# Kernel optimization log

Hardware: AMD Instinct MI355X
Metric: run time of the kernel (lower is better)

## Reference

```python
import jax, jax.numpy as jnp
import numpy as np

HEADS, K = 8, 32
EPS = 1e-5


def bn(x, gamma, beta):
    # batch-stat BN over all axes except the last (channel) axis
    axes = tuple(range(x.ndim - 1))
    m = jnp.mean(x, axes, keepdims=True)
    v = jnp.var(x, axes, keepdims=True)
    return (x - m) / jnp.sqrt(v + EPS) * gamma + beta


def leaky(z):
    return jax.nn.leaky_relu(z, 0.2)


def conv1(t, W, g, b):  # 1x1 Conv1d + BN + LeakyReLU, channels-last
    return leaky(bn(jnp.einsum('bnc,dc->bnd', t, W), g, b))


def conv2(t, W, g, b):  # 1x1 Conv2d + BN + LeakyReLU on (B,N,k,C)
    return leaky(bn(jnp.einsum('bnkc,dc->bnkd', t, W), g, b))


def _forward(x, pos, Wq, gq, bq, Wk, gk, bk, Wv, gv, bv,
             Wpb, gpb, bpb, We1, ge1, be1, We2, ge2, be2,
             Wm1, gm1, bm1, Wm2, gm2, bm2):
    B, N, C = x.shape
    cph = C // HEADS
    q = conv1(x, Wq, gq, bq)
    key = conv1(x, Wk, gk, bk)
    val = conv1(x, Wv, gv, bv)
    # kNN in key-feature space (DGCNN-style get_graph_feature, edge_function='global')
    sq = jnp.sum(key * key, -1)                          # (B,N)
    dist = sq[:, :, None] + sq[:, None, :] - 2.0 * jnp.einsum('bnc,bmc->bnm', key, key)
    _, idx = jax.lax.top_k(-dist, K)                     # (B,N,K)
    bidx = jnp.arange(B)[:, None, None]
    key_nb = key[bidx, idx]                              # (B,N,K,C)
    val_nb = val[bidx, idx]
    pos_nb = pos[bidx, idx]
    mask = jnp.sign(idx + 1).astype(x.dtype)             # (B,N,K), all ones for valid knn
    masked_pos = (pos_nb - pos[:, :, None, :]) * mask[..., None]
    posb = conv2(masked_pos, Wpb, gpb, bpb)              # (B,N,K,C)
    vector = key_nb - q[:, :, None, :] + posb            # vector attention logits input
    value = val_nb + posb
    vector = conv2(conv2(vector, We1, ge1, be1), We2, ge2, be2)  # (B,N,K,cph)
    vector = jax.nn.softmax(vector, axis=2) * mask[..., None]    # softmax over k neighbors
    value = value.reshape(B, N, K, cph, HEADS)
    attn = jnp.einsum('bnkgh,bnkg->bngh', value, vector).reshape(B, N, C)
    x = x + attn
    h = jax.nn.silu(bn(jnp.einsum('bnc,dc->bnd', x, Wm1), gm1, bm1))
    m = jax.nn.silu(bn(jnp.einsum('bnc,dc->bnd', h, Wm2), gm2, bm2))
    return x + m


def setup_inputs():
    key = jax.random.key(0)
    ks = jax.random.split(key, 16)
    B, N, C, H = 2, 2048, 256, 512
    cph = C // HEADS
    s = 0.02
    inp = {
        'x': jax.random.normal(ks[0], (B, N, C), jnp.float32),
        'pos': jax.random.normal(ks[1], (B, N, C), jnp.float32),
        'Wq': jax.random.normal(ks[2], (C, C), jnp.float32) * s,
        'gq': jnp.ones((C,), jnp.float32), 'bq': jnp.zeros((C,), jnp.float32),
        'Wk': jax.random.normal(ks[3], (C, C), jnp.float32) * s,
        'gk': jnp.ones((C,), jnp.float32), 'bk': jnp.zeros((C,), jnp.float32),
        'Wv': jax.random.normal(ks[4], (C, C), jnp.float32) * s,
        'gv': jnp.ones((C,), jnp.float32), 'bv': jnp.zeros((C,), jnp.float32),
        'Wpb': jax.random.normal(ks[5], (C, C), jnp.float32) * s,
        'gpb': jnp.ones((C,), jnp.float32), 'bpb': jnp.zeros((C,), jnp.float32),
        'We1': jax.random.normal(ks[6], (cph, C), jnp.float32) * s,
        'ge1': jnp.ones((cph,), jnp.float32), 'be1': jnp.zeros((cph,), jnp.float32),
        'We2': jax.random.normal(ks[7], (cph, cph), jnp.float32) * s,
        'ge2': jnp.ones((cph,), jnp.float32), 'be2': jnp.zeros((cph,), jnp.float32),
        'Wm1': jax.random.normal(ks[8], (H, C), jnp.float32) * s,
        'gm1': jnp.ones((H,), jnp.float32), 'bm1': jnp.zeros((H,), jnp.float32),
        'Wm2': jax.random.normal(ks[9], (C, H), jnp.float32) * s,
        'gm2': jnp.ones((C,), jnp.float32), 'bm2': jnp.zeros((C,), jnp.float32),
    }
    return inp


def reference(x, pos, Wq, gq, bq, Wk, gk, bk, Wv, gv, bv,
              Wpb, gpb, bpb, We1, ge1, be1, We2, ge2, be2,
              Wm1, gm1, bm1, Wm2, gm2, bm2):
    return _forward(x, pos, Wq, gq, bq, Wk, gk, bk, Wv, gv, bv,
                    Wpb, gpb, bpb, We1, ge1, be1, We2, ge2, be2,
                    Wm1, gm1, bm1, Wm2, gm2, bm2)
```

## Files before the change

kernel.cpp:

```cpp
#include <hip/hip_runtime.h>

#define EPS 1e-5f

typedef __attribute__((ext_vector_type(8))) short s8v;
typedef __attribute__((ext_vector_type(4))) float f4v;

__device__ __forceinline__ float leakyf(float z){ return z >= 0.f ? z : 0.2f*z; }
__device__ __forceinline__ float siluf(float y){ return y / (1.f + __expf(-y)); }
__device__ __forceinline__ unsigned f2bfu(float f){
  unsigned u = __float_as_uint(f);
  return (u + 0x7FFFu + ((u>>16)&1u)) >> 16;
}
__device__ __forceinline__ unsigned short bfr(float f){ return (unsigned short)f2bfu(f); }
__device__ __forceinline__ float bf2f16(unsigned short s){ return __uint_as_float(((unsigned)s)<<16); }

__global__ __launch_bounds__(256) void k_zero(float* __restrict__ p, int n){
  int i = blockIdx.x*256 + threadIdx.x;
  if (i < n) p[i] = 0.f;
}

template<bool TRANSA, bool STATS>
__global__ __launch_bounds__(256) void k_gemm(
    const float* __restrict__ A, int lda,
    const float* __restrict__ tA, const float* __restrict__ gA, const float* __restrict__ bA, int CA,
    const float* __restrict__ B0, const float* __restrict__ B1, const float* __restrict__ B2,
    int ldb, float* __restrict__ C, int ldc, long cStr, int K,
    float* __restrict__ buck, int statC, int statChanStr)
{
  __shared__ unsigned short Ah[2048], Al[2048], Bh[2048], Bl[2048];
  __shared__ float Ssum[64], Ssq[64];
  const int z = blockIdx.z;
  const float* Bb = (z==0?B0:(z==1?B1:B2));
  float* Cb = C + (long)z*cStr;
  const int tid = threadIdx.x;
  const int bm = blockIdx.x*64, bn = blockIdx.y*64;
  const int wv = tid>>6, lane = tid&63;
  const int lm = lane&15, quad = lane>>4;
  if (STATS && tid<64){ Ssum[tid]=0.f; Ssq[tid]=0.f; }

  const int r0 = tid>>3, kg = tid&7;
  const int qk = kg>>1, j0 = (kg&1)*4;
  const int s0 = ((((r0>>4)  )*4 + qk)*16 + ((r0&15)^qk))*8 + j0;
  const int s1 = ((((r0>>4)+2)*4 + qk)*16 + ((r0&15)^qk))*8 + j0;
  const float* aP0 = A  + (long)(bm+r0)*lda + kg*4;
  const float* aP1 = aP0 + (long)32*lda;
  const float* bP0 = Bb + (long)(bn+r0)*ldb + kg*4;
  const float* bP1 = bP0 + (long)32*ldb;

  f4v acc[4];
  #pragma unroll
  for (int j=0;j<4;j++) acc[j] = (f4v){0.f,0.f,0.f,0.f};

  float4 a0 = *(const float4*)(aP0);
  float4 a1 = *(const float4*)(aP1);
  float4 b0 = *(const float4*)(bP0);
  float4 b1 = *(const float4*)(bP1);

  for (int k0=0; k0<K; k0+=32){
    float4 av0 = a0, av1 = a1;
    if (TRANSA){
      const float* tm = tA + k0 + kg*4;
      float4 m4 = *(const float4*)tm;
      float4 r4 = *(const float4*)(tm + CA);
      float4 g4 = *(const float4*)(gA + k0 + kg*4);
      float4 b4 = *(const float4*)(bA + k0 + kg*4);
      av0.x = siluf((av0.x - m4.x)*r4.x*g4.x + b4.x);
      av0.y = siluf((av0.y - m4.y)*r4.y*g4.y + b4.y);
      av0.z = siluf((av0.z - m4.z)*r4.z*g4.z + b4.z);
      av0.w = siluf((av0.w - m4.w)*r4.w*g4.w + b4.w);
      av1.x = siluf((av1.x - m4.x)*r4.x*g4.x + b4.x);
      av1.y = siluf((av1.y - m4.y)*r4.y*g4.y + b4.y);
      av1.z = siluf((av1.z - m4.z)*r4.z*g4.z + b4.z);
      av1.w = siluf((av1.w - m4.w)*r4.w*g4.w + b4.w);
    }
    ushort4 h4, l4;
    h4.x=bfr(av0.x); l4.x=bfr(av0.x-bf2f16(h4.x));
    h4.y=bfr(av0.y); l4.y=bfr(av0.y-bf2f16(h4.y));
    h4.z=bfr(av0.z); l4.z=bfr(av0.z-bf2f16(h4.z));
    h4.w=bfr(av0.w); l4.w=bfr(av0.w-bf2f16(h4.w));
    *(ushort4*)&Ah[s0]=h4; *(ushort4*)&Al[s0]=l4;
    h4.x=bfr(av1.x); l4.x=bfr(av1.x-bf2f16(h4.x));
    h4.y=bfr(av1.y); l4.y=bfr(av1.y-bf2f16(h4.y));
    h4.z=bfr(av1.z); l4.z=bfr(av1.z-bf2f16(h4.z));
    h4.w=bfr(av1.w); l4.w=bfr(av1.w-bf2f16(h4.w));
    *(ushort4*)&Ah[s1]=h4; *(ushort4*)&Al[s1]=l4;
    h4.x=bfr(b0.x); l4.x=bfr(b0.x-bf2f16(h4.x));
    h4.y=bfr(b0.y); l4.y=bfr(b0.y-bf2f16(h4.y));
    h4.z=bfr(b0.z); l4.z=bfr(b0.z-bf2f16(h4.z));
    h4.w=bfr(b0.w); l4.w=bfr(b0.w-bf2f16(h4.w));
    *(ushort4*)&Bh[s0]=h4; *(ushort4*)&Bl[s0]=l4;
    h4.x=bfr(b1.x); l4.x=bfr(b1.x-bf2f16(h4.x));
    h4.y=bfr(b1.y); l4.y=bfr(b1.y-bf2f16(h4.y));
    h4.z=bfr(b1.z); l4.z=bfr(b1.z-bf2f16(h4.z));
    h4.w=bfr(b1.w); l4.w=bfr(b1.w-bf2f16(h4.w));
    *(ushort4*)&Bh[s1]=h4; *(ushort4*)&Bl[s1]=l4;
    __syncthreads();
    if (k0+32 < K){
      a0 = *(const float4*)(aP0 + k0+32);
      a1 = *(const float4*)(aP1 + k0+32);
      b0 = *(const float4*)(bP0 + k0+32);
      b1 = *(const float4*)(bP1 + k0+32);
    }
    const int soA = ((wv*4 + quad)*16 + (lm^quad))*8;
    s8v ah = *(const s8v*)&Ah[soA];
    s8v al = *(const s8v*)&Al[soA];
    #pragma unroll
    for (int j=0;j<4;j++){
      const int soB = ((j*4 + quad)*16 + (lm^quad))*8;
      s8v bh = *(const s8v*)&Bh[soB];
      s8v bl = *(const s8v*)&Bl[soB];
      acc[j] = __builtin_amdgcn_mfma_f32_16x16x32_bf16(ah, bh, acc[j], 0,0,0);
      acc[j] = __builtin_amdgcn_mfma_f32_16x16x32_bf16(ah, bl, acc[j], 0,0,0);
      acc[j] = __builtin_amdgcn_mfma_f32_16x16x32_bf16(al, bh, acc[j], 0,0,0);
      acc[j] = __builtin_amdgcn_mfma_f32_16x16x32_bf16(al, bl, acc[j], 0,0,0);
    }
    __syncthreads();
  }
  #pragma unroll
  for (int rr=0;rr<4;rr++){
    float* cr = Cb + (long)(bm + wv*16 + quad*4 + rr)*ldc + bn + lm;
    #pragma unroll
    for (int j=0;j<4;j++) cr[j*16] = acc[j][rr];
  }
  if (STATS){
    #pragma unroll
    for (int j=0;j<4;j++){
      float s=0.f, q=0.f;
      #pragma unroll
      for (int rr=0;rr<4;rr++){ float v = acc[j][rr]; s += v; q += v*v; }
      s += __shfl_xor(s,16,64); s += __shfl_xor(s,32,64);
      q += __shfl_xor(q,16,64); q += __shfl_xor(q,32,64);
      if (quad==0){ atomicAdd(&Ssum[j*16+lm], s); atomicAdd(&Ssq[j*16+lm], q); }
    }
    __syncthreads();
    if (tid < 64){
      int chan = statChanStr*z + bn + tid;
      float* bb = buck + (long)(blockIdx.x & 63)*2*statC;
      atomicAdd(&bb[chan], Ssum[tid]);
      atomicAdd(&bb[statC + chan], Ssq[tid]);
    }
  }
}

__global__ void k_finalize(const float* __restrict__ buck, int C, float invn, float* __restrict__ mr){
  int c = blockIdx.x*256 + threadIdx.x;
  if (c < C){
    float s=0,q=0;
    for (int b=0;b<64;b++){ s += buck[(long)b*2*C + c]; q += buck[(long)b*2*C + C + c]; }
    float m = s*invn;
    float v = fmaxf(q*invn - m*m, 0.f);
    mr[c] = m; mr[C+c] = rsqrtf(v + EPS);
  }
}

__global__ __launch_bounds__(256) void k_apply_qkv(const float* __restrict__ raw, const float* __restrict__ mr,
    const float* __restrict__ gq, const float* __restrict__ bq,
    const float* __restrict__ gk, const float* __restrict__ bk,
    const float* __restrict__ gv, const float* __restrict__ bv,
    float* __restrict__ key, float* __restrict__ qv, float* __restrict__ sq){
  const int r = blockIdx.x, tid = threadIdx.x;
  __shared__ float red[256];
  const float* row = raw + (long)r*768;
  float zq = row[tid], zk = row[256+tid], zv = row[512+tid];
  float yq = leakyf((zq - mr[tid])*mr[768+tid]*gq[tid] + bq[tid]);
  float yk = leakyf((zk - mr[256+tid])*mr[1024+tid]*gk[tid] + bk[tid]);
  float yv = leakyf((zv - mr[512+tid])*mr[1280+tid]*gv[tid] + bv[tid]);
  qv[(long)r*512 + tid] = yq;
  key[(long)r*256 + tid] = yk;
  qv[(long)r*512 + 256 + tid] = yv;
  red[tid] = yk*yk; __syncthreads();
  for (int off=128; off; off>>=1){ if (tid<off) red[tid] += red[tid+off]; __syncthreads(); }
  if (tid==0) sq[r] = red[0];
}

__global__ __launch_bounds__(256) void k_topk(const float* __restrict__ G, const float* __restrict__ sqb,
    int* __restrict__ idxb){
  __shared__ float dist[4][2048];
  const int wv = threadIdx.x >> 6, lane = threadIdx.x & 63;
  const int n = blockIdx.x*4 + wv;
  const float* Grow = G + (long)n*2048;
  const float sqn = sqb[n];
  float lmin = 3.4e38f; int lidx = 0;
  for (int j=0;j<32;j++){
    int m = lane + j*64;
    float d = sqn + sqb[m] - 2.f*Grow[m];
    dist[wv][m] = d;
    if (d < lmin){ lmin = d; lidx = m; }
  }
  int* orow = idxb + n*32;
  for (int t=0;t<32;t++){
    float v = lmin; int i = lidx;
    for (int off=32; off; off>>=1){
      float v2 = __shfl_xor(v, off, 64);
      int i2 = __shfl_xor(i, off, 64);
      if (v2 < v || (v2 == v && i2 < i)){ v = v2; i = i2; }
    }
    if (lane == 0) orow[t] = i;
    if ((i & 63) == lane){
      dist[wv][i] = 3.4e38f;
      lmin = 3.4e38f; lidx = 0;
      for (int j=0;j<32;j++){
        int m = lane + j*64;
        float d = dist[wv][m];
        if (d < lmin){ lmin = d; lidx = m; }
      }
    }
  }
}

__global__ __launch_bounds__(256) void k_stats_pb(const float* __restrict__ P, const int* __restrict__ idx,
    float* __restrict__ buck){
  const int c = threadIdx.x;
  float s=0,q=0;
  for (int r = blockIdx.x; r < 4096; r += gridDim.x){
    const long base = (long)(r >> 11) << 11;
    const float pn = P[(long)r*256 + c];
    const int* ir = idx + r*32;
    for (int k=0;k<32;k++){
      int g = ir[k];
      float z = P[(base + g)*256 + c] - pn;
      s += z; q += z*z;
    }
  }
  float* bb = buck + (long)(blockIdx.x & 63)*512;
  atomicAdd(&bb[c], s); atomicAdd(&bb[256+c], q);
}

__global__ __launch_bounds__(256) void k_e1m(
    const float* __restrict__ key, const float* __restrict__ qv, const float* __restrict__ P,
    const int* __restrict__ idx, const float* __restrict__ mrPB,
    const float* __restrict__ gpb, const float* __restrict__ bpb,
    const float* __restrict__ We1, float* __restrict__ E1, float* __restrict__ buckE1)
{
  __shared__ unsigned short Ab[16384];
  __shared__ unsigned short Wb[8192];
  __shared__ float Ssum[32], Ssq[32];
  const int tid = threadIdx.x;
  const int wv = tid>>6, lane = tid&63;
  const int quad = lane>>4, lm = lane&15;
  const int bn0 = blockIdx.x*2;
  if (tid < 32){ Ssum[tid]=0.f; Ssq[tid]=0.f; }
  for (int e = tid; e < 8192; e += 256){
    int d = e >> 8, c = e & 255;
    int off = (((d>>4)*8 + (c>>5))*4 + ((c>>3)&3))*128 + (d&15)*8 + (c&7);
    Wb[off] = bfr(We1[e]);
  }
  {
    const int bn = bn0 + (wv>>1);
    const long base = (long)(bn >> 11) << 11;
    const int c4 = lane*4;
    float4 q4  = *(const float4*)(qv + (long)bn*512 + c4);
    float4 pn4 = *(const float4*)(P + (long)bn*256 + c4);
    float4 mp4 = *(const float4*)(mrPB + c4);
    float4 rp4 = *(const float4*)(mrPB + 256 + c4);
    float4 g4  = *(const float4*)(gpb + c4);
    float4 b4  = *(const float4*)(bpb + c4);
    const int ksc = c4>>5, quadc = (c4>>3)&3, jc = c4&7;
    for (int j = 0; j < 16; ++j){
      const int rloc = wv*16 + j;
      const int kk = rloc & 31;
      const int g = idx[bn*32 + kk];
      float4 kb = *(const float4*)(key + (base+g)*256 + c4);
      float4 pb = *(const float4*)(P + (base+g)*256 + c4);
      float o0 = kb.x - q4.x + leakyf((pb.x - pn4.x - mp4.x)*rp4.x*g4.x + b4.x);
      float o1 = kb.y - q4.y + leakyf((pb.y - pn4.y - mp4.y)*rp4.y*g4.y + b4.y);
      float o2 = kb.z - q4.z + leakyf((pb.z - pn4.z - mp4.z)*rp4.z*g4.z + b4.z);
      float o3 = kb.w - q4.w + leakyf((pb.w - pn4.w - mp4.w)*rp4.w*g4.w + b4.w);
      const int atile = rloc >> 4;
      const int slot = ((rloc & 15) ^ (ksc<<1) ^ quadc) & 15;
      const int off = ((atile*8 + ksc)*4 + quadc)*128 + slot*8 + jc;
      ushort4 u; u.x = bfr(o0); u.y = bfr(o1); u.z = bfr(o2); u.w = bfr(o3);
      *(ushort4*)&Ab[off] = u;
    }
  }
  __syncthreads();
  f4v acc0 = (f4v){0,0,0,0}, acc1 = (f4v){0,0,0,0};
  #pragma unroll
  for (int ks=0; ks<8; ks++){
    const int aslot = (lm ^ (ks<<1) ^ quad) & 15;
    s8v a  = *(const s8v*)&Ab[((wv*8 + ks)*4 + quad)*128 + aslot*8];
    s8v b0 = *(const s8v*)&Wb[((ks)*4 + quad)*128 + lm*8];
    s8v b1 = *(const s8v*)&Wb[((8 + ks)*4 + quad)*128 + lm*8];
    acc0 = __builtin_amdgcn_mfma_f32_16x16x32_bf16(a, b0, acc0, 0,0,0);
    acc1 = __builtin_amdgcn_mfma_f32_16x16x32_bf16(a, b1, acc1, 0,0,0);
  }
  {
    const int bn = bn0 + (wv>>1);
    const int mt = wv & 1;
    #pragma unroll
    for (int rr=0; rr<4; rr++){
      int krow = mt*16 + quad*4 + rr;
      float* o = E1 + ((long)bn*32 + krow)*32;
      o[lm]      = acc0[rr];
      o[16 + lm] = acc1[rr];
    }
  }
  float s0=0,q0=0,s1=0,q1=0;
  #pragma unroll
  for (int rr=0; rr<4; rr++){
    s0 += acc0[rr]; q0 += acc0[rr]*acc0[rr];
    s1 += acc1[rr]; q1 += acc1[rr]*acc1[rr];
  }
  s0 += __shfl_xor(s0,16,64); s0 += __shfl_xor(s0,32,64);
  q0 += __shfl_xor(q0,16,64); q0 += __shfl_xor(q0,32,64);
  s1 += __shfl_xor(s1,16,64); s1 += __shfl_xor(s1,32,64);
  q1 += __shfl_xor(q1,16,64); q1 += __shfl_xor(q1,32,64);
  if (quad == 0){
    atomicAdd(&Ssum[lm], s0);      atomicAdd(&Ssq[lm], q0);
    atomicAdd(&Ssum[16+lm], s1);   atomicAdd(&Ssq[16+lm], q1);
  }
  __syncthreads();
  if (tid < 32){
    float* bb = buckE1 + (long)(blockIdx.x & 63)*64;
    atomicAdd(&bb[tid], Ssum[tid]); atomicAdd(&bb[32+tid], Ssq[tid]);
  }
}

__global__ __launch_bounds__(256) void k_e2m(
    float* __restrict__ E, const float* __restrict__ mrE1,
    const float* __restrict__ ge1, const float* __restrict__ be1,
    const float* __restrict__ We2, float* __restrict__ buckE2)
{
  __shared__ unsigned short Ab[8192];
  __shared__ unsigned short Wb[1024];
  __shared__ float Ssum[32], Ssq[32];
  const int tid = threadIdx.x;
  const int wv = tid>>6, lane = tid&63;
  const int quad = lane>>4, lm = lane&15;
  const long r0 = (long)blockIdx.x*256;
  if (tid < 32){ Ssum[tid]=0.f; Ssq[tid]=0.f; }
  for (int e = tid; e < 1024; e += 256){
    int d = e>>5, c = e&31;
    int off = ((d>>4)*4 + ((c>>3)&3))*128 + (d&15)*8 + (c&7);
    Wb[off] = bfr(We2[e]);
  }
  #pragma unroll
  for (int it=0; it<8; it++){
    int e = (tid + it*256)*4;
    int row = e>>5, c = e&31;
    float4 v = *(const float4*)(E + (r0 + row)*32 + c);
    float4 m4 = *(const float4*)(mrE1 + c);
    float4 r4 = *(const float4*)(mrE1 + 32 + c);
    float4 g4 = *(const float4*)(ge1 + c);
    float4 b4 = *(const float4*)(be1 + c);
    float o0 = leakyf((v.x - m4.x)*r4.x*g4.x + b4.x);
    float o1 = leakyf((v.y - m4.y)*r4.y*g4.y + b4.y);
    float o2 = leakyf((v.z - m4.z)*r4.z*g4.z + b4.z);
    float o3 = leakyf((v.w - m4.w)*r4.w*g4.w + b4.w);
    int quadc = (c>>3)&3, jc = c&7;
    int slot = ((row&15) ^ quadc) & 15;
    int off = ((row>>4)*4 + quadc)*128 + slot*8 + jc;
    ushort4 u; u.x=bfr(o0); u.y=bfr(o1); u.z=bfr(o2); u.w=bfr(o3);
    *(ushort4*)&Ab[off] = u;
  }
  __syncthreads();
  f4v acc0[4], acc1[4];
  #pragma unroll
  for (int i=0;i<4;i++){ acc0[i]=(f4v){0,0,0,0}; acc1[i]=(f4v){0,0,0,0}; }
  const int aslot = (lm ^ quad) & 15;
  s8v b0 = *(const s8v*)&Wb[(quad)*128 + lm*8];
  s8v b1 = *(const s8v*)&Wb[(4 + quad)*128 + lm*8];
  #pragma unroll
  for (int i=0;i<4;i++){
    const int atile = wv*4 + i;
    s8v a = *(const s8v*)&Ab[(atile*4 + quad)*128 + aslot*8];
    acc0[i] = __builtin_amdgcn_mfma_f32_16x16x32_bf16(a, b0, acc0[i], 0,0,0);
    acc1[i] = __builtin_amdgcn_mfma_f32_16x16x32_bf16(a, b1, acc1[i], 0,0,0);
  }
  __syncthreads();
  float s0=0,q0=0,s1=0,q1=0;
  #pragma unroll
  for (int i=0;i<4;i++){
    const int atile = wv*4 + i;
    #pragma unroll
    for (int rr=0; rr<4; rr++){
      long row = r0 + atile*16 + quad*4 + rr;
      float* o = E + row*32;
      o[lm]      = acc0[i][rr];
      o[16 + lm] = acc1[i][rr];
      s0 += acc0[i][rr]; q0 += acc0[i][rr]*acc0[i][rr];
      s1 += acc1[i][rr]; q1 += acc1[i][rr]*acc1[i][rr];
    }
  }
  s0 += __shfl_xor(s0,16,64); s0 += __shfl_xor(s0,32,64);
  q0 += __shfl_xor(q0,16,64); q0 += __shfl_xor(q0,32,64);
  s1 += __shfl_xor(s1,16,64); s1 += __shfl_xor(s1,32,64);
  q1 += __shfl_xor(q1,16,64); q1 += __shfl_xor(q1,32,64);
  if (quad == 0){
    atomicAdd(&Ssum[lm], s0);    atomicAdd(&Ssq[lm], q0);
    atomicAdd(&Ssum[16+lm], s1); atomicAdd(&Ssq[16+lm], q1);
  }
  __syncthreads();
  if (tid < 32){
    float* bb = buckE2 + (long)(blockIdx.x & 63)*64;
    atomicAdd(&bb[tid], Ssum[tid]); atomicAdd(&bb[32+tid], Ssq[tid]);
  }
}

__global__ __launch_bounds__(64) void k_attn(
    const float* __restrict__ E2, const float* __restrict__ mrE2,
    const float* __restrict__ ge2, const float* __restrict__ be2,
    const float* __restrict__ qv, const float* __restrict__ P, const int* __restrict__ idx,
    const float* __restrict__ mrPB, const float* __restrict__ gpb, const float* __restrict__ bpb,
    const float* __restrict__ xin, float* __restrict__ x2)
{
  __shared__ float L[32][33];
  const int lane = threadIdx.x;
  const int bn = blockIdx.x;
  const long base = (long)(bn >> 11) << 11;
  for (int qq=0; qq<4; qq++){
    int e = lane*16 + qq*4;
    int k = e >> 5, g0 = e & 31;
    float4 v  = *(const float4*)(E2 + (long)bn*1024 + e);
    float4 m4 = *(const float4*)(mrE2 + g0);
    float4 r4 = *(const float4*)(mrE2 + 32 + g0);
    float4 g4 = *(const float4*)(ge2 + g0);
    float4 b4 = *(const float4*)(be2 + g0);
    L[k][g0+0] = leakyf((v.x - m4.x)*r4.x*g4.x + b4.x);
    L[k][g0+1] = leakyf((v.y - m4.y)*r4.y*g4.y + b4.y);
    L[k][g0+2] = leakyf((v.z - m4.z)*r4.z*g4.z + b4.z);
    L[k][g0+3] = leakyf((v.w - m4.w)*r4.w*g4.w + b4.w);
  }
  __syncthreads();
  {
    const int g = lane & 31, h = lane >> 5;
    float mx = -3.4e38f;
    for (int j=0;j<16;j++) mx = fmaxf(mx, L[h*16+j][g]);
    mx = fmaxf(mx, __shfl_xor(mx, 32, 64));
    float sm = 0.f, ev[16];
    for (int j=0;j<16;j++){ float e_ = __expf(L[h*16+j][g] - mx); ev[j] = e_; sm += e_; }
    sm += __shfl_xor(sm, 32, 64);
    float inv = 1.f/sm;
    for (int j=0;j<16;j++) L[h*16+j][g] = ev[j]*inv;
  }
  __syncthreads();
  const int c4 = lane*4, gg = lane >> 1;
  float4 pn4 = *(const float4*)(P + (long)bn*256 + c4);
  float4 mp4 = *(const float4*)(mrPB + c4);
  float4 rp4 = *(const float4*)(mrPB + 256 + c4);
  float4 g4 = *(const float4*)(gpb + c4);
  float4 b4 = *(const float4*)(bpb + c4);
  float accv[4] = {0,0,0,0};
  const int* ir = idx + bn*32;
  for (int k=0;k<32;k++){
    int gi = ir[k];
    float4 vv = *(const float4*)(qv + (long)(base+gi)*512 + 256 + c4);
    float4 pp = *(const float4*)(P + (base+gi)*256 + c4);
    float w = L[k][gg];
    float zh0 = (pp.x - pn4.x - mp4.x)*rp4.x*g4.x + b4.x;
    float zh1 = (pp.y - pn4.y - mp4.y)*rp4.y*g4.y + b4.y;
    float zh2 = (pp.z - pn4.z - mp4.z)*rp4.z*g4.z + b4.z;
    float zh3 = (pp.w - pn4.w - mp4.w)*rp4.w*g4.w + b4.w;
    accv[0] = fmaf(vv.x + leakyf(zh0), w, accv[0]);
    accv[1] = fmaf(vv.y + leakyf(zh1), w, accv[1]);
    accv[2] = fmaf(vv.z + leakyf(zh2), w, accv[2]);
    accv[3] = fmaf(vv.w + leakyf(zh3), w, accv[3]);
  }
  float4 x4 = *(const float4*)(xin + (long)bn*256 + c4);
  float4 o;
  o.x = x4.x + accv[0]; o.y = x4.y + accv[1];
  o.z = x4.z + accv[2]; o.w = x4.w + accv[3];
  *(float4*)(x2 + (long)bn*256 + c4) = o;
}

__global__ __launch_bounds__(256) void k_final(const float* __restrict__ x2, const float* __restrict__ Zm2,
    const float* __restrict__ mr, const float* __restrict__ gm, const float* __restrict__ bm,
    float* __restrict__ out){
  const int r = blockIdx.x, c = threadIdx.x;
  float z = Zm2[(long)r*256 + c];
  float y = (z - mr[c])*mr[256+c]*gm[c] + bm[c];
  out[(long)r*256 + c] = x2[(long)r*256 + c] + siluf(y);
}

extern "C" void kernel_launch(void* const* d_in, const int* in_sizes, int n_in,
                              void* d_out, int out_size, void* d_ws, size_t ws_size,
                              hipStream_t stream){
  (void)in_sizes; (void)n_in; (void)out_size; (void)ws_size;
  const float* x   = (const float*)d_in[0];
  const float* pos = (const float*)d_in[1];
  const float* Wq  = (const float*)d_in[2];
  const float* gq  = (const float*)d_in[3];
  const float* bq  = (const float*)d_in[4];
  const float* Wk  = (const float*)d_in[5];
  const float* gk  = (const float*)d_in[6];
  const float* bk  = (const float*)d_in[7];
  const float* Wv  = (const float*)d_in[8];
  const float* gv  = (const float*)d_in[9];
  const float* bv  = (const float*)d_in[10];
  const float* Wpb = (const float*)d_in[11];
  const float* gpb = (const float*)d_in[12];
  const float* bpb = (const float*)d_in[13];
  const float* We1 = (const float*)d_in[14];
  const float* ge1 = (const float*)d_in[15];
  const float* be1 = (const float*)d_in[16];
  const float* We2 = (const float*)d_in[17];
  const float* ge2 = (const float*)d_in[18];
  const float* be2 = (const float*)d_in[19];
  const float* Wm1 = (const float*)d_in[20];
  const float* gm1 = (const float*)d_in[21];
  const float* bm1 = (const float*)d_in[22];
  const float* Wm2 = (const float*)d_in[23];
  const float* gm2 = (const float*)d_in[24];
  const float* bm2 = (const float*)d_in[25];

  float* w     = (float*)d_ws;
  float* arena = w;
  float* key   = w + 4194304;
  float* P     = w + 5242880;
  float* x2    = w + 6291456;
  float* qv    = w + 7340032;
  float* sq    = w + 9437184;
  int*   idx   = (int*)(w + 9441280);
  float* buck  = w + 9572352;
  float* mr    = w + 9809920;
  float* bQKV = buck;            float* bPB = buck + 98304;  float* bE1 = buck + 131072;
  float* bE2  = buck + 135168;   float* bM1 = buck + 139264; float* bM2 = buck + 204800;
  float* mrQKV = mr;        float* mrPB = mr + 1536; float* mrE1 = mr + 2048;
  float* mrE2  = mr + 2112; float* mrM1 = mr + 2176; float* mrM2 = mr + 3200;
  float* Zm1 = arena;
  float* Zm2 = arena + 2097152;

  k_zero<<<943,256,0,stream>>>(buck, 241280);
  k_gemm<false,true><<<dim3(64,4,3),256,0,stream>>>(x,256, nullptr,nullptr,nullptr,0,
      Wq,Wk,Wv,256, arena,768,256, 256, bQKV,768,256);
  k_gemm<false,false><<<dim3(64,4,1),256,0,stream>>>(pos,256, nullptr,nullptr,nullptr,0,
      Wpb,Wpb,Wpb,256, P,256,0, 256, nullptr,0,0);
  k_finalize<<<3,256,0,stream>>>(bQKV, 768, 1.f/4096.f, mrQKV);
  k_apply_qkv<<<4096,256,0,stream>>>(arena, mrQKV, gq,bq,gk,bk,gv,bv, key, qv, sq);
  k_gemm<false,false><<<dim3(32,32,1),256,0,stream>>>(key,256, nullptr,nullptr,nullptr,0,
      key,key,key,256, arena,2048,0, 256, nullptr,0,0);
  k_topk<<<512,256,0,stream>>>(arena, sq, idx);
  k_gemm<false,false><<<dim3(32,32,1),256,0,stream>>>(key+524288,256, nullptr,nullptr,nullptr,0,
      key+524288,key+524288,key+524288,256, arena,2048,0, 256, nullptr,0,0);
  k_topk<<<512,256,0,stream>>>(arena, sq+2048, idx+65536);
  k_stats_pb<<<256,256,0,stream>>>(P, idx, bPB);
  k_finalize<<<1,256,0,stream>>>(bPB, 256, 1.f/131072.f, mrPB);
  k_e1m<<<2048,256,0,stream>>>(key, qv, P, idx, mrPB, gpb, bpb, We1, arena, bE1);
  k_finalize<<<1,256,0,stream>>>(bE1, 32, 1.f/131072.f, mrE1);
  k_e2m<<<512,256,0,stream>>>(arena, mrE1, ge1, be1, We2, bE2);
  k_finalize<<<1,256,0,stream>>>(bE2, 32, 1.f/131072.f, mrE2);
  k_attn<<<4096,64,0,stream>>>(arena, mrE2, ge2, be2, qv, P, idx, mrPB, gpb, bpb, x, x2);
  k_gemm<false,true><<<dim3(64,8,1),256,0,stream>>>(x2,256, nullptr,nullptr,nullptr,0,
      Wm1,Wm1,Wm1,256, Zm1,512,0, 256, bM1,512,0);
  k_finalize<<<2,256,0,stream>>>(bM1, 512, 1.f/4096.f, mrM1);
  k_gemm<true,true><<<dim3(64,4,1),256,0,stream>>>(Zm1,512, mrM1,gm1,bm1,512,
      Wm2,Wm2,Wm2,512, Zm2,256,0, 512, bM2,256,0);
  k_finalize<<<1,256,0,stream>>>(bM2, 256, 1.f/4096.f, mrM2);
  k_final<<<4096,256,0,stream>>>(x2, Zm2, mrM2, gm2, bm2, (float*)d_out);
}
```

Measured before the change: 396.1 us.

## Fold BN finalize into consumers, merge pos GEMM into QKV launch, widen blocks

Removes four separate k_finalize launches by having each consumer kernel (k_gemm TRANSA path, k_e2m, k_attn, k_final) reduce the 64 stat buckets itself into shared memory. The pos/Wpb GEMM becomes a fourth z-slice of the QKV GEMM launch. k_attn now handles four points per 256-thread block, and k_final four rows per block. k_stats_pb gets more blocks. This cuts launch count and tail overhead, but every block now redundantly re-reads and reduces the bucket arrays.

New measurement: 372.6 us. -5.9%, faster.

```diff
diff --git a/kernel.cpp b/kernel.cpp
--- a/kernel.cpp
+++ b/kernel.cpp
@@ -22,28 +22,48 @@
 template<bool TRANSA, bool STATS>
 __global__ __launch_bounds__(256) void k_gemm(
     const float* __restrict__ A, int lda,
-    const float* __restrict__ tA, const float* __restrict__ gA, const float* __restrict__ bA, int CA,
-    const float* __restrict__ B0, const float* __restrict__ B1, const float* __restrict__ B2,
-    int ldb, float* __restrict__ C, int ldc, long cStr, int K,
-    float* __restrict__ buck, int statC, int statChanStr)
+    const float* __restrict__ A3, int lda3,
+    const float* __restrict__ fAbuck, float invnA, int CA,
+    const float* __restrict__ gA, const float* __restrict__ bA,
+    const float* __restrict__ B0, const float* __restrict__ B1,
+    const float* __restrict__ B2, const float* __restrict__ B3, int ldb,
+    float* __restrict__ C, int ldc, long cStr,
+    float* __restrict__ C3, int ldc3,
+    int K, float* __restrict__ buck, int statC, int statChanStr)
 {
   __shared__ unsigned short Ah[2048], Al[2048], Bh[2048], Bl[2048];
   __shared__ float Ssum[64], Ssq[64];
+  __shared__ float mrA[1024];
   const int z = blockIdx.z;
-  const float* Bb = (z==0?B0:(z==1?B1:B2));
-  float* Cb = C + (long)z*cStr;
+  const bool zAlt = (A3 != nullptr) && (z == 3);
+  const float* Az = zAlt ? A3 : A;
+  const int ldaz = zAlt ? lda3 : lda;
+  const float* Bb = (z==0?B0 : z==1?B1 : (z==2?B2:B3));
+  float* Cb = zAlt ? C3 : (C + (long)z*cStr);
+  const int ldcz = zAlt ? ldc3 : ldc;
+  const bool doStats = STATS && !zAlt;
   const int tid = threadIdx.x;
   const int bm = blockIdx.x*64, bn = blockIdx.y*64;
   const int wv = tid>>6, lane = tid&63;
   const int lm = lane&15, quad = lane>>4;
-  if (STATS && tid<64){ Ssum[tid]=0.f; Ssq[tid]=0.f; }
+  if (doStats && tid<64){ Ssum[tid]=0.f; Ssq[tid]=0.f; }
+  if (TRANSA){
+    for (int c = tid; c < CA; c += 256){
+      float s=0.f, q=0.f;
+      for (int b=0;b<64;b++){ s += fAbuck[(long)b*2*CA + c]; q += fAbuck[(long)b*2*CA + CA + c]; }
+      float m = s*invnA;
+      float v = fmaxf(q*invnA - m*m, 0.f);
+      mrA[c] = m; mrA[CA + c] = rsqrtf(v + EPS);
+    }
+    __syncthreads();
+  }
 
   const int r0 = tid>>3, kg = tid&7;
   const int qk = kg>>1, j0 = (kg&1)*4;
   const int s0 = ((((r0>>4)  )*4 + qk)*16 + ((r0&15)^qk))*8 + j0;
   const int s1 = ((((r0>>4)+2)*4 + qk)*16 + ((r0&15)^qk))*8 + j0;
-  const float* aP0 = A  + (long)(bm+r0)*lda + kg*4;
-  const float* aP1 = aP0 + (long)32*lda;
+  const float* aP0 = Az + (long)(bm+r0)*ldaz + kg*4;
+  const float* aP1 = aP0 + (long)32*ldaz;
   const float* bP0 = Bb + (long)(bn+r0)*ldb + kg*4;
   const float* bP1 = bP0 + (long)32*ldb;
 
@@ -59,9 +79,8 @@
   for (int k0=0; k0<K; k0+=32){
     float4 av0 = a0, av1 = a1;
     if (TRANSA){
-      const float* tm = tA + k0 + kg*4;
-      float4 m4 = *(const float4*)tm;
-      float4 r4 = *(const float4*)(tm + CA);
+      float4 m4 = *(const float4*)&mrA[k0 + kg*4];
+      float4 r4 = *(const float4*)&mrA[CA + k0 + kg*4];
       float4 g4 = *(const float4*)(gA + k0 + kg*4);
       float4 b4 = *(const float4*)(bA + k0 + kg*4);
       av0.x = siluf((av0.x - m4.x)*r4.x*g4.x + b4.x);
@@ -118,11 +137,11 @@
   }
   #pragma unroll
   for (int rr=0;rr<4;rr++){
-    float* cr = Cb + (long)(bm + wv*16 + quad*4 + rr)*ldc + bn + lm;
+    float* cr = Cb + (long)(bm + wv*16 + quad*4 + rr)*ldcz + bn + lm;
     #pragma unroll
     for (int j=0;j<4;j++) cr[j*16] = acc[j][rr];
   }
-  if (STATS){
+  if (doStats){
     #pragma unroll
     for (int j=0;j<4;j++){
       float s=0.f, q=0.f;
@@ -317,30 +336,39 @@
 }
 
 __global__ __launch_bounds__(256) void k_e2m(
-    float* __restrict__ E, const float* __restrict__ mrE1,
+    float* __restrict__ E, const float* __restrict__ bE1buck,
     const float* __restrict__ ge1, const float* __restrict__ be1,
     const float* __restrict__ We2, float* __restrict__ buckE2)
 {
   __shared__ unsigned short Ab[8192];
   __shared__ unsigned short Wb[1024];
   __shared__ float Ssum[32], Ssq[32];
+  __shared__ float mrE1s[64];
   const int tid = threadIdx.x;
   const int wv = tid>>6, lane = tid&63;
   const int quad = lane>>4, lm = lane&15;
   const long r0 = (long)blockIdx.x*256;
-  if (tid < 32){ Ssum[tid]=0.f; Ssq[tid]=0.f; }
+  if (tid < 32){
+    Ssum[tid]=0.f; Ssq[tid]=0.f;
+    float s=0.f, q=0.f;
+    for (int b=0;b<64;b++){ s += bE1buck[b*64+tid]; q += bE1buck[b*64+32+tid]; }
+    float m = s*(1.f/131072.f);
+    float v = fmaxf(q*(1.f/131072.f) - m*m, 0.f);
+    mrE1s[tid] = m; mrE1s[32+tid] = rsqrtf(v + EPS);
+  }
   for (int e = tid; e < 1024; e += 256){
     int d = e>>5, c = e&31;
     int off = ((d>>4)*4 + ((c>>3)&3))*128 + (d&15)*8 + (c&7);
     Wb[off] = bfr(We2[e]);
   }
+  __syncthreads();
   #pragma unroll
   for (int it=0; it<8; it++){
     int e = (tid + it*256)*4;
     int row = e>>5, c = e&31;
     float4 v = *(const float4*)(E + (r0 + row)*32 + c);
-    float4 m4 = *(const float4*)(mrE1 + c);
-    float4 r4 = *(const float4*)(mrE1 + 32 + c);
+    float4 m4 = *(const float4*)&mrE1s[c];
+    float4 r4 = *(const float4*)&mrE1s[32+c];
     float4 g4 = *(const float4*)(ge1 + c);
     float4 b4 = *(const float4*)(be1 + c);
     float o0 = leakyf((v.x - m4.x)*r4.x*g4.x + b4.x);
@@ -397,41 +425,51 @@
   }
 }
 
-__global__ __launch_bounds__(64) void k_attn(
-    const float* __restrict__ E2, const float* __restrict__ mrE2,
+__global__ __launch_bounds__(256) void k_attn(
+    const float* __restrict__ E2, const float* __restrict__ bE2buck,
     const float* __restrict__ ge2, const float* __restrict__ be2,
     const float* __restrict__ qv, const float* __restrict__ P, const int* __restrict__ idx,
     const float* __restrict__ mrPB, const float* __restrict__ gpb, const float* __restrict__ bpb,
     const float* __restrict__ xin, float* __restrict__ x2)
 {
-  __shared__ float L[32][33];
-  const int lane = threadIdx.x;
-  const int bn = blockIdx.x;
+  __shared__ float L[4][32][33];
+  __shared__ float mrE2s[64];
+  const int tid = threadIdx.x;
+  const int wv = tid>>6, lane = tid&63;
+  if (tid < 32){
+    float s=0.f, q=0.f;
+    for (int b=0;b<64;b++){ s += bE2buck[b*64+tid]; q += bE2buck[b*64+32+tid]; }
+    float m = s*(1.f/131072.f);
+    float v = fmaxf(q*(1.f/131072.f) - m*m, 0.f);
+    mrE2s[tid] = m; mrE2s[32+tid] = rsqrtf(v + EPS);
+  }
+  __syncthreads();
+  const int bn = blockIdx.x*4 + wv;
   const long base = (long)(bn >> 11) << 11;
   for (int qq=0; qq<4; qq++){
     int e = lane*16 + qq*4;
     int k = e >> 5, g0 = e & 31;
     float4 v  = *(const float4*)(E2 + (long)bn*1024 + e);
-    float4 m4 = *(const float4*)(mrE2 + g0);
-    float4 r4 = *(const float4*)(mrE2 + 32 + g0);
+    float4 m4 = *(const float4*)&mrE2s[g0];
+    float4 r4 = *(const float4*)&mrE2s[32+g0];
     float4 g4 = *(const float4*)(ge2 + g0);
     float4 b4 = *(const float4*)(be2 + g0);
-    L[k][g0+0] = leakyf((v.x - m4.x)*r4.x*g4.x + b4.x);
-    L[k][g0+1] = leakyf((v.y - m4.y)*r4.y*g4.y + b4.y);
-    L[k][g0+2] = leakyf((v.z - m4.z)*r4.z*g4.z + b4.z);
-    L[k][g0+3] = leakyf((v.w - m4.w)*r4.w*g4.w + b4.w);
+    L[wv][k][g0+0] = leakyf((v.x - m4.x)*r4.x*g4.x + b4.x);
+    L[wv][k][g0+1] = leakyf((v.y - m4.y)*r4.y*g4.y + b4.y);
+    L[wv][k][g0+2] = leakyf((v.z - m4.z)*r4.z*g4.z + b4.z);
+    L[wv][k][g0+3] = leakyf((v.w - m4.w)*r4.w*g4.w + b4.w);
   }
   __syncthreads();
   {
     const int g = lane & 31, h = lane >> 5;
     float mx = -3.4e38f;
-    for (int j=0;j<16;j++) mx = fmaxf(mx, L[h*16+j][g]);
+    for (int j=0;j<16;j++) mx = fmaxf(mx, L[wv][h*16+j][g]);
     mx = fmaxf(mx, __shfl_xor(mx, 32, 64));
     float sm = 0.f, ev[16];
-    for (int j=0;j<16;j++){ float e_ = __expf(L[h*16+j][g] - mx); ev[j] = e_; sm += e_; }
+    for (int j=0;j<16;j++){ float e_ = __expf(L[wv][h*16+j][g] - mx); ev[j] = e_; sm += e_; }
     sm += __shfl_xor(sm, 32, 64);
     float inv = 1.f/sm;
-    for (int j=0;j<16;j++) L[h*16+j][g] = ev[j]*inv;
+    for (int j=0;j<16;j++) L[wv][h*16+j][g] = ev[j]*inv;
   }
   __syncthreads();
   const int c4 = lane*4, gg = lane >> 1;
@@ -446,7 +484,7 @@
     int gi = ir[k];
     float4 vv = *(const float4*)(qv + (long)(base+gi)*512 + 256 + c4);
     float4 pp = *(const float4*)(P + (base+gi)*256 + c4);
-    float w = L[k][gg];
+    float w = L[wv][k][gg];
     float zh0 = (pp.x - pn4.x - mp4.x)*rp4.x*g4.x + b4.x;
     float zh1 = (pp.y - pn4.y - mp4.y)*rp4.y*g4.y + b4.y;
     float zh2 = (pp.z - pn4.z - mp4.z)*rp4.z*g4.z + b4.z;
@@ -464,12 +502,25 @@
 }
 
 __global__ __launch_bounds__(256) void k_final(const float* __restrict__ x2, const float* __restrict__ Zm2,
-    const float* __restrict__ mr, const float* __restrict__ gm, const float* __restrict__ bm,
+    const float* __restrict__ bM2buck, const float* __restrict__ gm, const float* __restrict__ bm,
     float* __restrict__ out){
-  const int r = blockIdx.x, c = threadIdx.x;
-  float z = Zm2[(long)r*256 + c];
-  float y = (z - mr[c])*mr[256+c]*gm[c] + bm[c];
-  out[(long)r*256 + c] = x2[(long)r*256 + c] + siluf(y);
+  __shared__ float mrs[512];
+  const int tid = threadIdx.x;
+  {
+    float s=0.f, q=0.f;
+    for (int b=0;b<64;b++){ s += bM2buck[(long)b*512 + tid]; q += bM2buck[(long)b*512 + 256 + tid]; }
+    float m = s*(1.f/4096.f);
+    float v = fmaxf(q*(1.f/4096.f) - m*m, 0.f);
+    mrs[tid] = m; mrs[256+tid] = rsqrtf(v + EPS);
+  }
+  __syncthreads();
+  #pragma unroll
+  for (int rr=0; rr<4; rr++){
+    long r = (long)blockIdx.x*4 + rr;
+    float z = Zm2[r*256 + tid];
+    float y = (z - mrs[tid])*mrs[256+tid]*gm[tid] + bm[tid];
+    out[r*256 + tid] = x2[r*256 + tid] + siluf(y);
+  }
 }
 
 extern "C" void kernel_launch(void* const* d_in, const int* in_sizes, int n_in,
@@ -515,36 +566,34 @@
   float* mr    = w + 9809920;
   float* bQKV = buck;            float* bPB = buck + 98304;  float* bE1 = buck + 131072;
   float* bE2  = buck + 135168;   float* bM1 = buck + 139264; float* bM2 = buck + 204800;
-  float* mrQKV = mr;        float* mrPB = mr + 1536; float* mrE1 = mr + 2048;
-  float* mrE2  = mr + 2112; float* mrM1 = mr + 2176; float* mrM2 = mr + 3200;
+  float* mrQKV = mr;        float* mrPB = mr + 1536;
   float* Zm1 = arena;
   float* Zm2 = arena + 2097152;
 
-  k_zero<<<943,256,0,stream>>>(buck, 241280);
-  k_gemm<false,true><<<dim3(64,4,3),256,0,stream>>>(x,256, nullptr,nullptr,nullptr,0,
-      Wq,Wk,Wv,256, arena,768,256, 256, bQKV,768,256);
-  k_gemm<false,false><<<dim3(64,4,1),256,0,stream>>>(pos,256, nullptr,nullptr,nullptr,0,
-      Wpb,Wpb,Wpb,256, P,256,0, 256, nullptr,0,0);
+  k_zero<<<928,256,0,stream>>>(buck, 237568);
+  k_gemm<false,true><<<dim3(64,4,4),256,0,stream>>>(
+      x,256, pos,256, nullptr,0.f,0, nullptr,nullptr,
+      Wq,Wk,Wv,Wpb,256, arena,768,256, P,256, 256, bQKV,768,256);
   k_finalize<<<3,256,0,stream>>>(bQKV, 768, 1.f/4096.f, mrQKV);
   k_apply_qkv<<<4096,256,0,stream>>>(arena, mrQKV, gq,bq,gk,bk,gv,bv, key, qv, sq);
-  k_gemm<false,false><<<dim3(32,32,1),256,0,stream>>>(key,256, nullptr,nullptr,nullptr,0,
-      key,key,key,256, arena,2048,0, 256, nullptr,0,0);
+  k_gemm<false,false><<<dim3(32,32,1),256,0,stream>>>(
+      key,256, nullptr,0, nullptr,0.f,0, nullptr,nullptr,
+      key,key,key,nullptr,256, arena,2048,0, nullptr,0, 256, nullptr,0,0);
   k_topk<<<512,256,0,stream>>>(arena, sq, idx);
-  k_gemm<false,false><<<dim3(32,32,1),256,0,stream>>>(key+524288,256, nullptr,nullptr,nullptr,0,
-      key+524288,key+524288,key+524288,256, arena,2048,0, 256, nullptr,0,0);
+  k_gemm<false,false><<<dim3(32,32,1),256,0,stream>>>(
+      key+524288,256, nullptr,0, nullptr,0.f,0, nullptr,nullptr,
+      key+524288,key+524288,key+524288,nullptr,256, arena,2048,0, nullptr,0, 256, nullptr,0,0);
   k_topk<<<512,256,0,stream>>>(arena, sq+2048, idx+65536);
-  k_stats_pb<<<256,256,0,stream>>>(P, idx, bPB);
+  k_stats_pb<<<1024,256,0,stream>>>(P, idx, bPB);
   k_finalize<<<1,256,0,stream>>>(bPB, 256, 1.f/131072.f, mrPB);
   k_e1m<<<2048,256,0,stream>>>(key, qv, P, idx, mrPB, gpb, bpb, We1, arena, bE1);
-  k_finalize<<<1,256,0,stream>>>(bE1, 32, 1.f/131072.f, mrE1);
-  k_e2m<<<512,256,0,stream>>>(arena, mrE1, ge1, be1, We2, bE2);
-  k_finalize<<<1,256,0,stream>>>(bE2, 32, 1.f/131072.f, mrE2);
-  k_attn<<<4096,64,0,stream>>>(arena, mrE2, ge2, be2, qv, P, idx, mrPB, gpb, bpb, x, x2);
-  k_gemm<false,true><<<dim3(64,8,1),256,0,stream>>>(x2,256, nullptr,nullptr,nullptr,0,
-      Wm1,Wm1,Wm1,256, Zm1,512,0, 256, bM1,512,0);
-  k_finalize<<<2,256,0,stream>>>(bM1, 512, 1.f/4096.f, mrM1);
-  k_gemm<true,true><<<dim3(64,4,1),256,0,stream>>>(Zm1,512, mrM1,gm1,bm1,512,
-      Wm2,Wm2,Wm2,512, Zm2,256,0, 512, bM2,256,0);
-  k_finalize<<<1,256,0,stream>>>(bM2, 256, 1.f/4096.f, mrM2);
-  k_final<<<4096,256,0,stream>>>(x2, Zm2, mrM2, gm2, bm2, (float*)d_out);
-}
+  k_e2m<<<512,256,0,stream>>>(arena, bE1, ge1, be1, We2, bE2);
+  k_attn<<<1024,256,0,stream>>>(arena, bE2, ge2, be2, qv, P, idx, mrPB, gpb, bpb, x, x2);
+  k_gemm<false,true><<<dim3(64,8,1),256,0,stream>>>(
+      x2,256, nullptr,0, nullptr,0.f,0, nullptr,nullptr,
+      Wm1,Wm1,Wm1,nullptr,256, Zm1,512,0, nullptr,0, 256, bM1,512,0);
+  k_gemm<true,true><<<dim3(64,4,1),256,0,stream>>>(
+      Zm1,512, nullptr,0, bM1,1.f/4096.f,512, gm1,bm1,
+      Wm2,Wm2,Wm2,nullptr,512, Zm2,256,0, nullptr,0, 512, bM2,256,0);
+  k_final<<<1024,256,0,stream>>>(x2, Zm2, bM2, gm2, bm2, (float*)d_out);
+}
```
